# Kernel tuning notes

Hardware: AMD Instinct MI355X
Metric: run time of the kernel (lower is better)

The kernel has to match this reference:

```python
import jax, jax.numpy as jnp
import numpy as np

N = 4096
IN_DIM, HID, OUT_DIM = 512, 256, 64
PROP_STEP = 10
LAM_HAT = 0.9
SCAD_A = 3.7
EPS = 1e-8


def setup_inputs() -> dict:
    key = jax.random.key(0)
    kA, kF, k1, k2 = jax.random.split(key, 4)
    # sparse symmetric 0/1 adjacency, zero diagonal (add_loops adds I later)
    u = jax.random.uniform(kA, (N, N), dtype=jnp.float32)
    A = (u < 0.005).astype(jnp.float32)
    A = jnp.maximum(A, A.T)
    A = A * (1.0 - jnp.eye(N, dtype=jnp.float32))
    F = jax.random.normal(kF, (N, IN_DIM), dtype=jnp.float32)
    W1 = jax.random.normal(k1, (IN_DIM, HID), dtype=jnp.float32) / np.sqrt(IN_DIM)
    b1 = jnp.zeros((HID,), dtype=jnp.float32)
    W2 = jax.random.normal(k2, (HID, OUT_DIM), dtype=jnp.float32) / np.sqrt(HID)
    b2 = jnp.zeros((OUT_DIM,), dtype=jnp.float32)
    raw_gamma = jnp.zeros((PROP_STEP,), dtype=jnp.float32)
    return {"A": A, "F": F, "W1": W1, "b1": b1, "W2": W2, "b2": b2,
            "raw_gamma": raw_gamma}


def reference(A, F, W1, b1, W2, b2, raw_gamma):
    lam = 1.0 / LAM_HAT - 1.0
    a = SCAD_A
    # MLP (dropout inactive at inference)
    F0 = jax.nn.relu(F @ W1 + b1) @ W2 + b2            # [N, out_dim]
    eye = jnp.eye(A.shape[0], dtype=A.dtype)
    A = A + eye                                        # add_loops
    D = A.sum(-1)                                      # [N]
    D_sq = jnp.sqrt(D)[:, None]                        # [N, 1]
    A_tilde = A / D_sq / D_sq.T                        # sym_norm: D^-1/2 A D^-1/2
    gammas = jax.nn.sigmoid(raw_gamma) * 2.0           # per-layer gamma in (0, 2)

    def step(Fc, gamma_k):
        Fn = Fc / D_sq
        nrm = jnp.linalg.norm(Fn, axis=-1, keepdims=True)
        Fu = Fn / jnp.maximum(nrm, 1e-12)
        # cosine distance in [0, 2]; detached as in torch (.detach())
        y = jax.lax.stop_gradient(1.0 - Fu @ Fu.T)     # [N, N]
        lam_k = jnp.maximum(gamma_k / a, EPS)
        t = a * lam_k
        safe_y = jnp.where(y <= 0.0, 1.0, y)
        w_mid = (t - y) / ((a - 1.0) * safe_y)
        # SCAD weight: 1 for y<=lam_k, linear decay on [lam_k, a*lam_k], 0 beyond
        W = jnp.where(y <= lam_k, 1.0, jnp.where(y <= t, w_mid, 0.0))
        W = W * (1.0 - eye)
        W = jnp.where(jnp.isnan(W), 1.0, W)
        Q_hat = ((W * A).sum(-1) / D + lam)[:, None]   # [N, 1]
        F_new = (W * A_tilde) @ Fc / Q_hat + lam * F0 / Q_hat
        return F_new, None

    F_out, _ = jax.lax.scan(step, F0, gammas)
    return F_out
```

## Files before the change

### kernel.cpp

```cpp
#include <hip/hip_runtime.h>
#include <hip/hip_bf16.h>

#define N_NODES 4096
#define IN_DIM  512
#define HID_DIM 256
#define OUT_DIM 64
#define PROP_STEP 10
#define MAX_DEG 128
#define KSPLIT  4
#define MLP1_BLOCKS (64 * 4 * KSPLIT)
#define LAM_CONST (1.0f/0.9f - 1.0f)
#define SCAD_A 3.7f

__device__ __forceinline__ ushort f2bf(float f) {
    unsigned u = __float_as_uint(f);
    unsigned r = (u + 0x7FFFu + ((u >> 16) & 1u)) >> 16;
    return (ushort)r;
}
__device__ __forceinline__ unsigned pack2(float lo, float hi) {
    return (unsigned)f2bf(lo) | ((unsigned)f2bf(hi) << 16);
}
__device__ __forceinline__ float bflo(unsigned u) { return __uint_as_float(u << 16); }
__device__ __forceinline__ float bfhi(unsigned u) { return __uint_as_float(u & 0xFFFF0000u); }

__device__ __forceinline__ float wave_reduce_add(float v) {
#pragma unroll
    for (int off = 32; off > 0; off >>= 1) v += __shfl_xor(v, off, 64);
    return v;
}

__global__ __launch_bounds__(256) void build_mlp1(
    const float* __restrict__ A, const float* __restrict__ F,
    const float* __restrict__ W1, float* __restrict__ Hp,
    int* __restrict__ ell, int* __restrict__ deg,
    float* __restrict__ invD, float* __restrict__ invDsq)
{
    if (blockIdx.x < MLP1_BLOCKS) {
        __shared__ float sA[16][68];
        __shared__ float sB[16][68];
        int bid = blockIdx.x;
        int t  = threadIdx.x;
        int m0 = (bid & 63) * 64;
        int n0 = ((bid >> 6) & 3) * 64;
        int kp = bid >> 8;
        int tm = (t & 15) * 4;
        int tn = (t >> 4) * 4;
        int ar = t >> 2;
        int ac = (t & 3) * 4;
        int br = t >> 4;
        int bc = (t & 15) * 4;
        float acc[4][4] = {};
        int k0 = kp * (IN_DIM / KSPLIT);
        for (int kc = k0; kc < k0 + IN_DIM / KSPLIT; kc += 16) {
            float4 va = *(const float4*)(F  + (size_t)(m0 + ar) * IN_DIM + kc + ac);
            float4 vb = *(const float4*)(W1 + (size_t)(kc + br) * HID_DIM + n0 + bc);
            __syncthreads();
            sA[ac + 0][ar] = va.x;
            sA[ac + 1][ar] = va.y;
            sA[ac + 2][ar] = va.z;
            sA[ac + 3][ar] = va.w;
            *(float4*)&sB[br][bc] = vb;
            __syncthreads();
#pragma unroll
            for (int k = 0; k < 16; k++) {
                float4 a = *(const float4*)&sA[k][tm];
                float4 b = *(const float4*)&sB[k][tn];
                acc[0][0] += a.x * b.x; acc[0][1] += a.x * b.y; acc[0][2] += a.x * b.z; acc[0][3] += a.x * b.w;
                acc[1][0] += a.y * b.x; acc[1][1] += a.y * b.y; acc[1][2] += a.y * b.z; acc[1][3] += a.y * b.w;
                acc[2][0] += a.z * b.x; acc[2][1] += a.z * b.y; acc[2][2] += a.z * b.z; acc[2][3] += a.z * b.w;
                acc[3][0] += a.w * b.x; acc[3][1] += a.w * b.y; acc[3][2] += a.w * b.z; acc[3][3] += a.w * b.w;
            }
        }
        float* Hb = Hp + (size_t)kp * N_NODES * HID_DIM;
#pragma unroll
        for (int r = 0; r < 4; r++) {
            *(float4*)&Hb[(size_t)(m0 + tm + r) * HID_DIM + n0 + tn] =
                make_float4(acc[r][0], acc[r][1], acc[r][2], acc[r][3]);
        }
    } else {
        __shared__ int cnt;
        int i = blockIdx.x - MLP1_BLOCKS;
        int t = threadIdx.x;
        if (t == 0) cnt = 0;
        __syncthreads();
        const float4* row = (const float4*)(A + (size_t)i * N_NODES);
        for (int q = t; q < N_NODES / 4; q += 256) {
            float4 v = row[q];
            if (v.x != 0.0f) { int p = atomicAdd(&cnt, 1); if (p < MAX_DEG) ell[i * MAX_DEG + p] = q * 4 + 0; }
            if (v.y != 0.0f) { int p = atomicAdd(&cnt, 1); if (p < MAX_DEG) ell[i * MAX_DEG + p] = q * 4 + 1; }
            if (v.z != 0.0f) { int p = atomicAdd(&cnt, 1); if (p < MAX_DEG) ell[i * MAX_DEG + p] = q * 4 + 2; }
            if (v.w != 0.0f) { int p = atomicAdd(&cnt, 1); if (p < MAX_DEG) ell[i * MAX_DEG + p] = q * 4 + 3; }
        }
        __syncthreads();
        if (t == 0) {
            int c = cnt;
            if (c > MAX_DEG) c = MAX_DEG;
            deg[i] = c;
            int pad = (c + 15) & ~15;
            if (pad > MAX_DEG) pad = MAX_DEG;
            for (int p = c; p < pad; p++) ell[i * MAX_DEG + p] = i;
            float d = (float)(cnt + 1);
            invD[i] = 1.0f / d;
            invDsq[i] = rsqrtf(d);
        }
    }
}

__global__ __launch_bounds__(256) void mlp2r(
    const float* __restrict__ Hp, const float* __restrict__ b1,
    const float* __restrict__ W2, const float* __restrict__ b2,
    const float* __restrict__ invDsq,
    float* __restrict__ F0, unsigned* __restrict__ P0, float* __restrict__ nrm0)
{
    __shared__ float sW2[HID_DIM * OUT_DIM];
    __shared__ float hbuf[4][HID_DIM];
    int tid  = threadIdx.x;
    int wid  = tid >> 6, lane = tid & 63;
    int row  = blockIdx.x * 4 + wid;
    const size_t PS = (size_t)N_NODES * HID_DIM;

    for (int i = tid; i < HID_DIM * OUT_DIM / 4; i += 256)
        ((float4*)sW2)[i] = ((const float4*)W2)[i];

    const float* hrow = Hp + (size_t)row * HID_DIM + lane * 4;
    float4 s0 = *(const float4*)(hrow);
    float4 s1 = *(const float4*)(hrow + PS);
    float4 s2 = *(const float4*)(hrow + 2 * PS);
    float4 s3 = *(const float4*)(hrow + 3 * PS);
    float4 bb = *(const float4*)(b1 + lane * 4);
    float h0 = fmaxf(s0.x + s1.x + s2.x + s3.x + bb.x, 0.0f);
    float h1 = fmaxf(s0.y + s1.y + s2.y + s3.y + bb.y, 0.0f);
    float h2 = fmaxf(s0.z + s1.z + s2.z + s3.z + bb.z, 0.0f);
    float h3 = fmaxf(s0.w + s1.w + s2.w + s3.w + bb.w, 0.0f);
    __syncthreads();
    hbuf[wid][lane * 4 + 0] = h0;
    hbuf[wid][lane * 4 + 1] = h1;
    hbuf[wid][lane * 4 + 2] = h2;
    hbuf[wid][lane * 4 + 3] = h3;
    __syncthreads();

    float acc = b2[lane];
#pragma unroll 8
    for (int k = 0; k < HID_DIM; k++) {
        acc += hbuf[wid][k] * sW2[k * OUT_DIM + lane];
    }

    size_t o = (size_t)row * OUT_DIM + lane;
    F0[o] = acc;
    float fn = acc * invDsq[row];
    float nrm = fmaxf(sqrtf(wave_reduce_add(fn * fn)), 1e-12f);
    float fu = fn / nrm;
    float fu_hi = __shfl_xor(fu, 1, 64);
    if ((lane & 1) == 0) {
        P0[(size_t)row * 32 + (lane >> 1)] = pack2(fu, fu_hi);
    }
    if (lane == 0) nrm0[row] = nrm;
}

__global__ __launch_bounds__(64, 8) void propagate(
    const unsigned* __restrict__ Pin, const float* __restrict__ nrmIn,
    const float* __restrict__ F0,
    const int* __restrict__ ell, const int* __restrict__ deg,
    const float* __restrict__ invD, const float* __restrict__ invDsq,
    const float* __restrict__ raw_gamma, int step,
    unsigned* __restrict__ Pout, float* __restrict__ nrmOut,
    float* __restrict__ FcOut, int writeNext, int writeOut)
{
    int lane = threadIdx.x;
    int r    = blockIdx.x;
    int g    = lane >> 3;
    int sl   = lane & 7;
    const float inv_am1 = 1.0f / (SCAD_A - 1.0f);

    float gamma = 2.0f / (1.0f + expf(-raw_gamma[step]));
    float lam_k = fmaxf(gamma / SCAD_A, 1e-8f);
    float tt    = SCAD_A * lam_k;

    int dg = deg[r];
    int pad = (dg + 15) & ~15;
    int npair = pad >> 4;
    const int* nb = ell + (size_t)r * MAX_DEG;
    int ed0 = (lane < pad)      ? nb[lane]      : r;
    int ed1 = (64 + lane < pad) ? nb[64 + lane] : r;

    uint4 up = *(const uint4*)(Pin + (size_t)r * 32 + sl * 4);
    float ui[8] = { bflo(up.x), bfhi(up.x), bflo(up.y), bfhi(up.y),
                    bflo(up.z), bfhi(up.z), bflo(up.w), bfhi(up.w) };

    float acc[8] = {};
    float qsum = 0.0f;
    for (int it = 0; it < npair; ++it) {
        int e0 = it * 16 + g;
        int e1 = e0 + 8;
        int src = (it < 4) ? ed0 : ed1;
        int j0 = __shfl(src, e0 & 63, 64);
        int j1 = __shfl(src, e1 & 63, 64);
        uint4 u0 = *(const uint4*)(Pin + (size_t)j0 * 32 + sl * 4);
        uint4 u1 = *(const uint4*)(Pin + (size_t)j1 * 32 + sl * 4);
        float nr0 = nrmIn[j0];
        float nr1 = nrmIn[j1];

        float pa = ui[0] * bflo(u0.x) + ui[1] * bfhi(u0.x) + ui[2] * bflo(u0.y) + ui[3] * bfhi(u0.y)
                 + ui[4] * bflo(u0.z) + ui[5] * bfhi(u0.z) + ui[6] * bflo(u0.w) + ui[7] * bfhi(u0.w);
        float pb = ui[0] * bflo(u1.x) + ui[1] * bfhi(u1.x) + ui[2] * bflo(u1.y) + ui[3] * bfhi(u1.y)
                 + ui[4] * bflo(u1.z) + ui[5] * bfhi(u1.z) + ui[6] * bflo(u1.w) + ui[7] * bfhi(u1.w);
        pa += __shfl_xor(pa, 1, 64); pb += __shfl_xor(pb, 1, 64);
        pa += __shfl_xor(pa, 2, 64); pb += __shfl_xor(pb, 2, 64);
        pa += __shfl_xor(pa, 4, 64); pb += __shfl_xor(pb, 4, 64);
        float ya = 1.0f - pa, yb = 1.0f - pb;
        float wa = (ya <= lam_k) ? 1.0f : ((ya <= tt) ? (tt - ya) * inv_am1 / ya : 0.0f);
        float wb = (yb <= lam_k) ? 1.0f : ((yb <= tt) ? (tt - yb) * inv_am1 / yb : 0.0f);
        if (e0 >= dg) wa = 0.0f;
        if (e1 >= dg) wb = 0.0f;
        qsum += wa + wb;
        float wsa = wa * nr0;
        float wsb = wb * nr1;
        acc[0] += wsa * bflo(u0.x) + wsb * bflo(u1.x);
        acc[1] += wsa * bfhi(u0.x) + wsb * bfhi(u1.x);
        acc[2] += wsa * bflo(u0.y) + wsb * bflo(u1.y);
        acc[3] += wsa * bfhi(u0.y) + wsb * bfhi(u1.y);
        acc[4] += wsa * bflo(u0.z) + wsb * bflo(u1.z);
        acc[5] += wsa * bfhi(u0.z) + wsb * bfhi(u1.z);
        acc[6] += wsa * bflo(u0.w) + wsb * bflo(u1.w);
        acc[7] += wsa * bfhi(u0.w) + wsb * bfhi(u1.w);
    }

#pragma unroll
    for (int off = 8; off <= 32; off <<= 1) {
#pragma unroll
        for (int q = 0; q < 8; q++) acc[q] += __shfl_xor(acc[q], off, 64);
        qsum += __shfl_xor(qsum, off, 64);
    }

    float iDs = invDsq[r];
    float Qh  = qsum * invD[r] + LAM_CONST;
    float rQh = 1.0f / Qh;
    const float4* f04 = (const float4*)(F0 + (size_t)r * OUT_DIM + sl * 8);
    float4 f0a = f04[0], f0b = f04[1];
    float f0v[8] = { f0a.x, f0a.y, f0a.z, f0a.w, f0b.x, f0b.y, f0b.z, f0b.w };
    float res[8];
#pragma unroll
    for (int q = 0; q < 8; q++) res[q] = (acc[q] * iDs + LAM_CONST * f0v[q]) * rQh;

    if (writeOut && lane < 8) {
        float4* o4 = (float4*)(FcOut + (size_t)r * OUT_DIM + sl * 8);
        o4[0] = make_float4(res[0], res[1], res[2], res[3]);
        o4[1] = make_float4(res[4], res[5], res[6], res[7]);
    }
    if (writeNext) {
        float fn[8];
        float ssq = 0.0f;
#pragma unroll
        for (int q = 0; q < 8; q++) { fn[q] = res[q] * iDs; ssq += fn[q] * fn[q]; }
        ssq += __shfl_xor(ssq, 1, 64);
        ssq += __shfl_xor(ssq, 2, 64);
        ssq += __shfl_xor(ssq, 4, 64);
        float nrm = fmaxf(sqrtf(ssq), 1e-12f);
        float inv_n = 1.0f / nrm;
        if (lane < 8) {
            uint4 fuPk;
            fuPk.x = pack2(fn[0] * inv_n, fn[1] * inv_n);
            fuPk.y = pack2(fn[2] * inv_n, fn[3] * inv_n);
            fuPk.z = pack2(fn[4] * inv_n, fn[5] * inv_n);
            fuPk.w = pack2(fn[6] * inv_n, fn[7] * inv_n);
            *(uint4*)(Pout + (size_t)r * 32 + sl * 4) = fuPk;
        }
        if (lane == 0) nrmOut[r] = nrm;
    }
}

extern "C" void kernel_launch(void* const* d_in, const int* in_sizes, int n_in,
                              void* d_out, int out_size, void* d_ws, size_t ws_size,
                              hipStream_t stream)
{
    const float* A  = (const float*)d_in[0];
    const float* F  = (const float*)d_in[1];
    const float* W1 = (const float*)d_in[2];
    const float* b1 = (const float*)d_in[3];
    const float* W2 = (const float*)d_in[4];
    const float* b2 = (const float*)d_in[5];
    const float* rg = (const float*)d_in[6];
    float* out = (float*)d_out;

    char* p = (char*)d_ws;
    float* Hp     = (float*)p; p += (size_t)KSPLIT * N_NODES * HID_DIM * 4;
    float* F0     = (float*)p; p += (size_t)N_NODES * OUT_DIM * 4;
    unsigned* Pa  = (unsigned*)p; p += (size_t)N_NODES * 32 * 4;
    unsigned* Pb  = (unsigned*)p; p += (size_t)N_NODES * 32 * 4;
    float* nrmA   = (float*)p; p += (size_t)N_NODES * 4;
    float* nrmB   = (float*)p; p += (size_t)N_NODES * 4;
    float* invD   = (float*)p; p += (size_t)N_NODES * 4;
    float* invDsq = (float*)p; p += (size_t)N_NODES * 4;
    int*   deg    = (int*)p;   p += (size_t)N_NODES * 4;
    int*   ell    = (int*)p;   p += (size_t)N_NODES * MAX_DEG * 4;

    build_mlp1<<<MLP1_BLOCKS + N_NODES, 256, 0, stream>>>(
        A, F, W1, Hp, ell, deg, invD, invDsq);
    mlp2r<<<N_NODES / 4, 256, 0, stream>>>(Hp, b1, W2, b2, invDsq, F0, Pa, nrmA);

    for (int k = 0; k < PROP_STEP; k++) {
        unsigned* Pin   = (k & 1) ? Pb : Pa;
        unsigned* Pout  = (k & 1) ? Pa : Pb;
        float* nIn      = (k & 1) ? nrmB : nrmA;
        float* nOut     = (k & 1) ? nrmA : nrmB;
        int last = (k == PROP_STEP - 1);
        propagate<<<N_NODES, 64, 0, stream>>>(
            Pin, nIn, F0, ell, deg, invD, invDsq, rg, k,
            Pout, nOut, out, !last, last);
    }
}
```

Measured before the change: 213.8 us.

## Fuse propagation steps into one persistent kernel with grid barriers

Replaces the ten per-step propagate launches with a single persistent kernel of 256 blocks. Each wave owns four rows and keeps their neighbor lists, degrees and F0 values in registers across steps. Steps are separated by an atomic-counter grid barrier. This removes launch overhead and repeated loads of per-row metadata. In exchange it gets fewer waves in flight to hide gather latency, adds barrier spin cost, and depends on all 256 blocks being co-resident.

After: 657.1 us. +207.3%, slower.

```diff
diff --git a/kernel.cpp b/kernel.cpp
--- a/kernel.cpp
+++ b/kernel.cpp
@@ -9,6 +9,8 @@
 #define MAX_DEG 128
 #define KSPLIT  4
 #define MLP1_BLOCKS (64 * 4 * KSPLIT)
+#define PROP_BLOCKS 256
+#define ROWS_PER_WAVE 4
 #define LAM_CONST (1.0f/0.9f - 1.0f)
 #define SCAD_A 3.7f
 
@@ -27,6 +29,18 @@
 #pragma unroll
     for (int off = 32; off > 0; off >>= 1) v += __shfl_xor(v, off, 64);
     return v;
+}
+
+__device__ __forceinline__ void grid_barrier(int* cnt, int target) {
+    __threadfence();
+    __syncthreads();
+    if (threadIdx.x == 0) {
+        __hip_atomic_fetch_add(cnt, 1, __ATOMIC_ACQ_REL, __HIP_MEMORY_SCOPE_AGENT);
+        while (__hip_atomic_load(cnt, __ATOMIC_ACQUIRE, __HIP_MEMORY_SCOPE_AGENT) < target)
+            __builtin_amdgcn_s_sleep(2);
+    }
+    __syncthreads();
+    __threadfence();
 }
 
 __global__ __launch_bounds__(256) void build_mlp1(
@@ -157,115 +171,141 @@
     if (lane == 0) nrm0[row] = nrm;
 }
 
-__global__ __launch_bounds__(64, 8) void propagate(
-    const unsigned* __restrict__ Pin, const float* __restrict__ nrmIn,
+__global__ __launch_bounds__(256) void propagate_fused(
+    unsigned* __restrict__ Pa, unsigned* __restrict__ Pb,
+    float* __restrict__ nrmA, float* __restrict__ nrmB,
     const float* __restrict__ F0,
     const int* __restrict__ ell, const int* __restrict__ deg,
     const float* __restrict__ invD, const float* __restrict__ invDsq,
-    const float* __restrict__ raw_gamma, int step,
-    unsigned* __restrict__ Pout, float* __restrict__ nrmOut,
-    float* __restrict__ FcOut, int writeNext, int writeOut)
+    const float* __restrict__ raw_gamma, float* __restrict__ out,
+    int* __restrict__ gcnt)
 {
-    int lane = threadIdx.x;
-    int r    = blockIdx.x;
+    int tid  = threadIdx.x;
+    int wid  = tid >> 6, lane = tid & 63;
     int g    = lane >> 3;
     int sl   = lane & 7;
+    int rbase = blockIdx.x * (4 * ROWS_PER_WAVE) + wid * ROWS_PER_WAVE;
     const float inv_am1 = 1.0f / (SCAD_A - 1.0f);
 
-    float gamma = 2.0f / (1.0f + expf(-raw_gamma[step]));
-    float lam_k = fmaxf(gamma / SCAD_A, 1e-8f);
-    float tt    = SCAD_A * lam_k;
-
-    int dg = deg[r];
-    int pad = (dg + 15) & ~15;
-    int npair = pad >> 4;
-    const int* nb = ell + (size_t)r * MAX_DEG;
-    int ed0 = (lane < pad)      ? nb[lane]      : r;
-    int ed1 = (64 + lane < pad) ? nb[64 + lane] : r;
-
-    uint4 up = *(const uint4*)(Pin + (size_t)r * 32 + sl * 4);
-    float ui[8] = { bflo(up.x), bfhi(up.x), bflo(up.y), bfhi(up.y),
-                    bflo(up.z), bfhi(up.z), bflo(up.w), bfhi(up.w) };
-
-    float acc[8] = {};
-    float qsum = 0.0f;
-    for (int it = 0; it < npair; ++it) {
-        int e0 = it * 16 + g;
-        int e1 = e0 + 8;
-        int src = (it < 4) ? ed0 : ed1;
-        int j0 = __shfl(src, e0 & 63, 64);
-        int j1 = __shfl(src, e1 & 63, 64);
-        uint4 u0 = *(const uint4*)(Pin + (size_t)j0 * 32 + sl * 4);
-        uint4 u1 = *(const uint4*)(Pin + (size_t)j1 * 32 + sl * 4);
-        float nr0 = nrmIn[j0];
-        float nr1 = nrmIn[j1];
-
-        float pa = ui[0] * bflo(u0.x) + ui[1] * bfhi(u0.x) + ui[2] * bflo(u0.y) + ui[3] * bfhi(u0.y)
-                 + ui[4] * bflo(u0.z) + ui[5] * bfhi(u0.z) + ui[6] * bflo(u0.w) + ui[7] * bfhi(u0.w);
-        float pb = ui[0] * bflo(u1.x) + ui[1] * bfhi(u1.x) + ui[2] * bflo(u1.y) + ui[3] * bfhi(u1.y)
-                 + ui[4] * bflo(u1.z) + ui[5] * bfhi(u1.z) + ui[6] * bflo(u1.w) + ui[7] * bfhi(u1.w);
-        pa += __shfl_xor(pa, 1, 64); pb += __shfl_xor(pb, 1, 64);
-        pa += __shfl_xor(pa, 2, 64); pb += __shfl_xor(pb, 2, 64);
-        pa += __shfl_xor(pa, 4, 64); pb += __shfl_xor(pb, 4, 64);
-        float ya = 1.0f - pa, yb = 1.0f - pb;
-        float wa = (ya <= lam_k) ? 1.0f : ((ya <= tt) ? (tt - ya) * inv_am1 / ya : 0.0f);
-        float wb = (yb <= lam_k) ? 1.0f : ((yb <= tt) ? (tt - yb) * inv_am1 / yb : 0.0f);
-        if (e0 >= dg) wa = 0.0f;
-        if (e1 >= dg) wb = 0.0f;
-        qsum += wa + wb;
-        float wsa = wa * nr0;
-        float wsb = wb * nr1;
-        acc[0] += wsa * bflo(u0.x) + wsb * bflo(u1.x);
-        acc[1] += wsa * bfhi(u0.x) + wsb * bfhi(u1.x);
-        acc[2] += wsa * bflo(u0.y) + wsb * bflo(u1.y);
-        acc[3] += wsa * bfhi(u0.y) + wsb * bfhi(u1.y);
-        acc[4] += wsa * bflo(u0.z) + wsb * bflo(u1.z);
-        acc[5] += wsa * bfhi(u0.z) + wsb * bfhi(u1.z);
-        acc[6] += wsa * bflo(u0.w) + wsb * bflo(u1.w);
-        acc[7] += wsa * bfhi(u0.w) + wsb * bfhi(u1.w);
-    }
-
-#pragma unroll
-    for (int off = 8; off <= 32; off <<= 1) {
-#pragma unroll
-        for (int q = 0; q < 8; q++) acc[q] += __shfl_xor(acc[q], off, 64);
-        qsum += __shfl_xor(qsum, off, 64);
-    }
-
-    float iDs = invDsq[r];
-    float Qh  = qsum * invD[r] + LAM_CONST;
-    float rQh = 1.0f / Qh;
-    const float4* f04 = (const float4*)(F0 + (size_t)r * OUT_DIM + sl * 8);
-    float4 f0a = f04[0], f0b = f04[1];
-    float f0v[8] = { f0a.x, f0a.y, f0a.z, f0a.w, f0b.x, f0b.y, f0b.z, f0b.w };
-    float res[8];
-#pragma unroll
-    for (int q = 0; q < 8; q++) res[q] = (acc[q] * iDs + LAM_CONST * f0v[q]) * rQh;
-
-    if (writeOut && lane < 8) {
-        float4* o4 = (float4*)(FcOut + (size_t)r * OUT_DIM + sl * 8);
-        o4[0] = make_float4(res[0], res[1], res[2], res[3]);
-        o4[1] = make_float4(res[4], res[5], res[6], res[7]);
-    }
-    if (writeNext) {
-        float fn[8];
-        float ssq = 0.0f;
-#pragma unroll
-        for (int q = 0; q < 8; q++) { fn[q] = res[q] * iDs; ssq += fn[q] * fn[q]; }
-        ssq += __shfl_xor(ssq, 1, 64);
-        ssq += __shfl_xor(ssq, 2, 64);
-        ssq += __shfl_xor(ssq, 4, 64);
-        float nrm = fmaxf(sqrtf(ssq), 1e-12f);
-        float inv_n = 1.0f / nrm;
-        if (lane < 8) {
-            uint4 fuPk;
-            fuPk.x = pack2(fn[0] * inv_n, fn[1] * inv_n);
-            fuPk.y = pack2(fn[2] * inv_n, fn[3] * inv_n);
-            fuPk.z = pack2(fn[4] * inv_n, fn[5] * inv_n);
-            fuPk.w = pack2(fn[6] * inv_n, fn[7] * inv_n);
-            *(uint4*)(Pout + (size_t)r * 32 + sl * 4) = fuPk;
-        }
-        if (lane == 0) nrmOut[r] = nrm;
+    int   dgA[ROWS_PER_WAVE], npA[ROWS_PER_WAVE];
+    int   e0A[ROWS_PER_WAVE], e1A[ROWS_PER_WAVE];
+    float iDA[ROWS_PER_WAVE], iDsA[ROWS_PER_WAVE], f0A[ROWS_PER_WAVE][8];
+#pragma unroll
+    for (int m = 0; m < ROWS_PER_WAVE; m++) {
+        int r = rbase + m;
+        int dg = deg[r];
+        dgA[m] = dg;
+        int pad = (dg + 15) & ~15;
+        npA[m] = pad >> 4;
+        const int* nb = ell + (size_t)r * MAX_DEG;
+        e0A[m] = (lane < pad)      ? nb[lane]      : r;
+        e1A[m] = (64 + lane < pad) ? nb[64 + lane] : r;
+        iDA[m]  = invD[r];
+        iDsA[m] = invDsq[r];
+        const float4* f04 = (const float4*)(F0 + (size_t)r * OUT_DIM + sl * 8);
+        float4 fa = f04[0], fb = f04[1];
+        f0A[m][0] = fa.x; f0A[m][1] = fa.y; f0A[m][2] = fa.z; f0A[m][3] = fa.w;
+        f0A[m][4] = fb.x; f0A[m][5] = fb.y; f0A[m][6] = fb.z; f0A[m][7] = fb.w;
+    }
+
+    for (int k = 0; k < PROP_STEP; k++) {
+        const unsigned* __restrict__ Pin = (k & 1) ? Pb : Pa;
+        unsigned* __restrict__ Pout      = (k & 1) ? Pa : Pb;
+        const float* __restrict__ nIn    = (k & 1) ? nrmB : nrmA;
+        float* __restrict__ nOut         = (k & 1) ? nrmA : nrmB;
+        float gamma = 2.0f / (1.0f + expf(-raw_gamma[k]));
+        float lam_k = fmaxf(gamma / SCAD_A, 1e-8f);
+        float tt    = SCAD_A * lam_k;
+
+        for (int m = 0; m < ROWS_PER_WAVE; m++) {
+            int r = rbase + m;
+            uint4 up = *(const uint4*)(Pin + (size_t)r * 32 + sl * 4);
+            float ui[8] = { bflo(up.x), bfhi(up.x), bflo(up.y), bfhi(up.y),
+                            bflo(up.z), bfhi(up.z), bflo(up.w), bfhi(up.w) };
+            float acc[8] = {};
+            float qsum = 0.0f;
+            int dg = dgA[m], npair = npA[m];
+            int ed0 = e0A[m], ed1 = e1A[m];
+            for (int it = 0; it < npair; ++it) {
+                int e0 = it * 16 + g;
+                int e1 = e0 + 8;
+                int src = (it < 4) ? ed0 : ed1;
+                int j0 = __shfl(src, e0 & 63, 64);
+                int j1 = __shfl(src, e1 & 63, 64);
+                uint4 u0 = *(const uint4*)(Pin + (size_t)j0 * 32 + sl * 4);
+                uint4 u1 = *(const uint4*)(Pin + (size_t)j1 * 32 + sl * 4);
+                float nr0 = nIn[j0];
+                float nr1 = nIn[j1];
+
+                float pa = ui[0] * bflo(u0.x) + ui[1] * bfhi(u0.x) + ui[2] * bflo(u0.y) + ui[3] * bfhi(u0.y)
+                         + ui[4] * bflo(u0.z) + ui[5] * bfhi(u0.z) + ui[6] * bflo(u0.w) + ui[7] * bfhi(u0.w);
+                float pb = ui[0] * bflo(u1.x) + ui[1] * bfhi(u1.x) + ui[2] * bflo(u1.y) + ui[3] * bfhi(u1.y)
+                         + ui[4] * bflo(u1.z) + ui[5] * bfhi(u1.z) + ui[6] * bflo(u1.w) + ui[7] * bfhi(u1.w);
+                pa += __shfl_xor(pa, 1, 64); pb += __shfl_xor(pb, 1, 64);
+                pa += __shfl_xor(pa, 2, 64); pb += __shfl_xor(pb, 2, 64);
+                pa += __shfl_xor(pa, 4, 64); pb += __shfl_xor(pb, 4, 64);
+                float ya = 1.0f - pa, yb = 1.0f - pb;
+                float wa = (ya <= lam_k) ? 1.0f : ((ya <= tt) ? (tt - ya) * inv_am1 / ya : 0.0f);
+                float wb = (yb <= lam_k) ? 1.0f : ((yb <= tt) ? (tt - yb) * inv_am1 / yb : 0.0f);
+                if (e0 >= dg) wa = 0.0f;
+                if (e1 >= dg) wb = 0.0f;
+                qsum += wa + wb;
+                float wsa = wa * nr0;
+                float wsb = wb * nr1;
+                acc[0] += wsa * bflo(u0.x) + wsb * bflo(u1.x);
+                acc[1] += wsa * bfhi(u0.x) + wsb * bfhi(u1.x);
+                acc[2] += wsa * bflo(u0.y) + wsb * bflo(u1.y);
+                acc[3] += wsa * bfhi(u0.y) + wsb * bfhi(u1.y);
+                acc[4] += wsa * bflo(u0.z) + wsb * bflo(u1.z);
+                acc[5] += wsa * bfhi(u0.z) + wsb * bfhi(u1.z);
+                acc[6] += wsa * bflo(u0.w) + wsb * bflo(u1.w);
+                acc[7] += wsa * bfhi(u0.w) + wsb * bfhi(u1.w);
+            }
+
+#pragma unroll
+            for (int off = 8; off <= 32; off <<= 1) {
+#pragma unroll
+                for (int q = 0; q < 8; q++) acc[q] += __shfl_xor(acc[q], off, 64);
+                qsum += __shfl_xor(qsum, off, 64);
+            }
+
+            float iDs = iDsA[m];
+            float Qh  = qsum * iDA[m] + LAM_CONST;
+            float rQh = 1.0f / Qh;
+            float res[8];
+#pragma unroll
+            for (int q = 0; q < 8; q++) res[q] = (acc[q] * iDs + LAM_CONST * f0A[m][q]) * rQh;
+
+            if (k == PROP_STEP - 1) {
+                if (lane < 8) {
+                    float4* o4 = (float4*)(out + (size_t)r * OUT_DIM + sl * 8);
+                    o4[0] = make_float4(res[0], res[1], res[2], res[3]);
+                    o4[1] = make_float4(res[4], res[5], res[6], res[7]);
+                }
+            } else {
+                float fn[8];
+                float ssq = 0.0f;
+#pragma unroll
+                for (int q = 0; q < 8; q++) { fn[q] = res[q] * iDs; ssq += fn[q] * fn[q]; }
+                ssq += __shfl_xor(ssq, 1, 64);
+                ssq += __shfl_xor(ssq, 2, 64);
+                ssq += __shfl_xor(ssq, 4, 64);
+                float nrm = fmaxf(sqrtf(ssq), 1e-12f);
+                float inv_n = 1.0f / nrm;
+                if (lane < 8) {
+                    uint4 fuPk;
+                    fuPk.x = pack2(fn[0] * inv_n, fn[1] * inv_n);
+                    fuPk.y = pack2(fn[2] * inv_n, fn[3] * inv_n);
+                    fuPk.z = pack2(fn[4] * inv_n, fn[5] * inv_n);
+                    fuPk.w = pack2(fn[6] * inv_n, fn[7] * inv_n);
+                    *(uint4*)(Pout + (size_t)r * 32 + sl * 4) = fuPk;
+                }
+                if (lane == 0) nOut[r] = nrm;
+            }
+        }
+        if (k < PROP_STEP - 1) {
+            grid_barrier(gcnt, (k + 1) * PROP_BLOCKS);
+        }
     }
 }
 
@@ -293,19 +333,14 @@
     float* invDsq = (float*)p; p += (size_t)N_NODES * 4;
     int*   deg    = (int*)p;   p += (size_t)N_NODES * 4;
     int*   ell    = (int*)p;   p += (size_t)N_NODES * MAX_DEG * 4;
+    int*   gcnt   = (int*)p;   p += 128;
+
+    hipMemsetAsync(gcnt, 0, 128, stream);
 
     build_mlp1<<<MLP1_BLOCKS + N_NODES, 256, 0, stream>>>(
         A, F, W1, Hp, ell, deg, invD, invDsq);
     mlp2r<<<N_NODES / 4, 256, 0, stream>>>(Hp, b1, W2, b2, invDsq, F0, Pa, nrmA);
 
-    for (int k = 0; k < PROP_STEP; k++) {
-        unsigned* Pin   = (k & 1) ? Pb : Pa;
-        unsigned* Pout  = (k & 1) ? Pa : Pb;
-        float* nIn      = (k & 1) ? nrmB : nrmA;
-        float* nOut     = (k & 1) ? nrmA : nrmB;
-        int last = (k == PROP_STEP - 1);
-        propagate<<<N_NODES, 64, 0, stream>>>(
-            Pin, nIn, F0, ell, deg, invD, invDsq, rg, k,
-            Pout, nOut, out, !last, last);
-    }
-}
+    propagate_fused<<<PROP_BLOCKS, 256, 0, stream>>>(
+        Pa, Pb, nrmA, nrmB, F0, ell, deg, invD, invDsq, rg, out, gcnt);
+}
```
